# Optimization experiments

Measured on AMD Instinct MI355X. Metric: run time of the kernel, lower is better.

The kernel has to match this reference:

```python
import jax, jax.numpy as jnp
import numpy as np

N_NODES = 100000


def gcn_conv(x, W, b, row, col, n_nodes):
    # Symmetric GCN normalization without self-loops (add_self_loops=False):
    # deg[i] = number of incoming edges at target i (edge_weight = 1)
    deg = jax.ops.segment_sum(jnp.ones(row.shape[0], dtype=x.dtype), col,
                              num_segments=n_nodes)
    dinv = jnp.where(deg > 0, jax.lax.rsqrt(jnp.maximum(deg, 1.0)), 0.0)
    norm = dinv[row] * dinv[col]  # [E]
    h = x @ W                      # [N, out] linear transform first (PyG order)
    msg = h[row] * norm[:, None]   # gather + scale, [E, out]
    out = jax.ops.segment_sum(msg, col, num_segments=n_nodes)  # scatter-add
    return out + b


def setup_inputs() -> dict:
    key = jax.random.key(0)
    k1, k2, k3, k4, k5, k6 = jax.random.split(key, 6)
    n, in_c, hid, out_c, e = N_NODES, 128, 32, 16, 3200000
    x = jax.random.normal(k1, (n, in_c), dtype=jnp.float32)
    edge_index = jax.random.randint(k2, (2, e), 0, n, dtype=jnp.int64)
    # Glorot-style init for GCN weights, zeros bias (PyG default)
    W1 = jax.random.normal(k3, (in_c, hid), dtype=jnp.float32) / np.sqrt(in_c)
    b1 = jnp.zeros((hid,), dtype=jnp.float32)
    W2 = jax.random.normal(k4, (hid, out_c), dtype=jnp.float32) / np.sqrt(hid)
    b2 = jnp.zeros((out_c,), dtype=jnp.float32)
    return {"x": x, "edge_index": edge_index, "W1": W1, "b1": b1,
            "W2": W2, "b2": b2}


def reference(x, edge_index, W1, b1, W2, b2):
    row, col = edge_index[0], edge_index[1]
    h = gcn_conv(x, W1, b1, row, col, N_NODES)
    h = jax.nn.relu(h)
    out = gcn_conv(h, W2, b2, row, col, N_NODES)
    return (out, 0)
```

## Files before the change

kernel.cpp:

```cpp
#include <hip/hip_runtime.h>


#define WAVE 64
#define BN2 512
#define NBMAX 256
#define CHUNK 8192

typedef _Float16 f16;

__global__ void bucket_count_kernel(const int* __restrict__ col, int* __restrict__ gcnt,
                                    int E, int nb) {
    __shared__ int h[NBMAX];
    for (int i = threadIdx.x; i < nb; i += blockDim.x) h[i] = 0;
    __syncthreads();
    for (int e = blockIdx.x * blockDim.x + threadIdx.x; e < E; e += gridDim.x * blockDim.x)
        atomicAdd(&h[col[e] >> 9], 1);
    __syncthreads();
    for (int i = threadIdx.x; i < nb; i += blockDim.x)
        if (h[i]) atomicAdd(&gcnt[i], h[i]);
}

__global__ void bucket_scan_kernel(const int* __restrict__ cnt, int* __restrict__ bptr,
                                   int* __restrict__ gcur, int nb, int* __restrict__ gpcur,
                                   f16* __restrict__ hA, f16* __restrict__ h2t, int nzr) {
    int lane = threadIdx.x;
    if (lane == 0) gpcur[0] = 0;
    if (lane < 32)      hA[(size_t)nzr * 32 + lane]         = (f16)0.f;
    else if (lane < 48) h2t[(size_t)nzr * 16 + (lane - 32)] = (f16)0.f;
    int carry = 0;
    for (int base = 0; base < nb; base += WAVE) {
        int i = base + lane;
        int orig = (i < nb) ? cnt[i] : 0;
        int v = orig;
#pragma unroll
        for (int off = 1; off < WAVE; off <<= 1) {
            int t = __shfl_up(v, off, WAVE);
            if (lane >= off) v += t;
        }
        if (i < nb) { bptr[i] = carry + v - orig; gcur[i] = carry + v - orig; }
        carry += __shfl(v, WAVE - 1, WAVE);
    }
    if (lane == 0) bptr[nb] = carry;
}

__global__ void __launch_bounds__(512)
partition_kernel(const int* __restrict__ row, const int* __restrict__ col,
                 int* __restrict__ gcursor, unsigned* __restrict__ packed,
                 int E, int nb) {
    __shared__ int hist[NBMAX], excl[NBMAX], cursor[NBMAX], baseoff[NBMAX];
    __shared__ unsigned stage[CHUNK];
    int chunk0 = blockIdx.x * CHUNK;
    int cn = E - chunk0; if (cn > CHUNK) cn = CHUNK;
    for (int i = threadIdx.x; i < nb; i += blockDim.x) hist[i] = 0;
    __syncthreads();
    for (int i = threadIdx.x; i < cn; i += blockDim.x)
        atomicAdd(&hist[col[chunk0 + i] >> 9], 1);
    __syncthreads();
    if (threadIdx.x < WAVE) {
        int lane = threadIdx.x, carry = 0;
        for (int base = 0; base < nb; base += WAVE) {
            int i = base + lane;
            int orig = (i < nb) ? hist[i] : 0;
            int v = orig;
#pragma unroll
            for (int off = 1; off < WAVE; off <<= 1) {
                int t = __shfl_up(v, off, WAVE);
                if (lane >= off) v += t;
            }
            if (i < nb) { excl[i] = carry + v - orig; cursor[i] = carry + v - orig; }
            carry += __shfl(v, WAVE - 1, WAVE);
        }
    }
    __syncthreads();
    for (int b = threadIdx.x; b < nb; b += blockDim.x) {
        int c = hist[b];
        baseoff[b] = c ? atomicAdd(&gcursor[b], c) : 0;
    }
    __syncthreads();
    for (int i = threadIdx.x; i < cn; i += blockDim.x) {
        int c = col[chunk0 + i], r = row[chunk0 + i];
        int b = c >> 9;
        int pos = atomicAdd(&cursor[b], 1);
        stage[pos] = ((unsigned)r << 9) | (unsigned)(c & (BN2 - 1));
    }
    __syncthreads();
    int wave = threadIdx.x >> 6, lane = threadIdx.x & 63, nw = blockDim.x >> 6;
    for (int b = wave; b < nb; b += nw) {
        int c = hist[b]; if (!c) continue;
        int s = excl[b], d = baseoff[b];
        for (int k = lane; k < c; k += WAVE) packed[d + k] = stage[s + k];
    }
}

__global__ void __launch_bounds__(512)
sort_kernel(const int* __restrict__ bptr, const unsigned* __restrict__ packed,
            int* __restrict__ srcs, int2* __restrict__ pse,
            float* __restrict__ dinv, int* __restrict__ gpcur,
            int n, int nb, int E) {
    __shared__ int hist[BN2], pex[BN2], cur[BN2];
    __shared__ int pbase_s;
    int b = blockIdx.x;
    int start = bptr[b], end = bptr[b + 1];
    for (int i = threadIdx.x; i < BN2; i += blockDim.x) { hist[i] = 0; cur[i] = 0; }
    __syncthreads();
    for (int k = start + threadIdx.x; k < end; k += blockDim.x)
        atomicAdd(&hist[packed[k] & (BN2 - 1)], 1);
    __syncthreads();
    if (threadIdx.x < WAVE) {
        int lane = threadIdx.x, carry = 0;
#pragma unroll
        for (int base = 0; base < BN2; base += WAVE) {
            int i = base + lane;
            int pd = (hist[i] + 15) & ~15;
            int v = pd;
#pragma unroll
            for (int off = 1; off < WAVE; off <<= 1) {
                int t = __shfl_up(v, off, WAVE);
                if (lane >= off) v += t;
            }
            pex[i] = carry + v - pd;
            carry += __shfl(v, WAVE - 1, WAVE);
        }
        if (lane == 0) pbase_s = atomicAdd(gpcur, carry);
    }
    __syncthreads();
    int pbase = pbase_s;
    for (int i = threadIdx.x; i < BN2; i += blockDim.x) {
        int node = b * BN2 + i;
        if (node < n) {
            int d = hist[i], pd = (d + 15) & ~15;
            int ps = pbase + pex[i];
            pse[node]  = d ? make_int2(ps, ps + pd) : make_int2(0, 0);
            dinv[node] = d ? rsqrtf((float)d) : 0.f;
            for (int k = d; k < pd; ++k) srcs[ps + k] = n;
        }
    }
    __syncthreads();
    for (int k = start + threadIdx.x; k < end; k += blockDim.x) {
        unsigned p = packed[k];
        int lc = p & (BN2 - 1);
        int pos = atomicAdd(&cur[lc], 1);
        srcs[pbase + pex[lc] + pos] = (int)(p >> 9);
    }
}

template <int INC, int OUTC, int JT>
__global__ void __launch_bounds__(256, 4)
dense_kernel(const float* __restrict__ x, const float* __restrict__ W,
             const float* __restrict__ dinv, f16* __restrict__ h, int n) {
    const int LSTR = INC + 4;
    const int SP   = 256 / JT;
    const int NT   = SP * 2;
    __shared__ float Wt[OUTC * LSTR];
    for (int i = threadIdx.x; i < INC * OUTC; i += 256) {
        int k = i / OUTC, j = i % OUTC;
        Wt[j * LSTR + k] = W[i];
    }
    __syncthreads();
    const int jg = threadIdx.x % JT;
    const int sp = threadIdx.x / JT;
    int base = blockIdx.x * NT;
    int n0 = base + sp;
    int n1 = base + sp + SP;
    int n0c = n0 < n ? n0 : n - 1;
    int n1c = n1 < n ? n1 : n - 1;
    const float4* xr0 = (const float4*)(x + (size_t)n0c * INC);
    const float4* xr1 = (const float4*)(x + (size_t)n1c * INC);
    float a[2][4] = {{0.f, 0.f, 0.f, 0.f}, {0.f, 0.f, 0.f, 0.f}};
#pragma unroll 4
    for (int k4 = 0; k4 < INC / 4; ++k4) {
        float4 v0 = xr0[k4];
        float4 v1 = xr1[k4];
#pragma unroll
        for (int u = 0; u < 4; ++u) {
            float4 w = *(const float4*)(Wt + (jg + u * JT) * LSTR + 4 * k4);
            a[0][u] = fmaf(v0.x, w.x, fmaf(v0.y, w.y, fmaf(v0.z, w.z, fmaf(v0.w, w.w, a[0][u]))));
            a[1][u] = fmaf(v1.x, w.x, fmaf(v1.y, w.y, fmaf(v1.z, w.z, fmaf(v1.w, w.w, a[1][u]))));
        }
    }
#pragma unroll
    for (int pair = 0; pair < 2; ++pair) {
        int nn = pair ? n1 : n0;
        if (nn < n) {
            float d = dinv[nn];
            f16* hr = h + (size_t)nn * OUTC;
#pragma unroll
            for (int u = 0; u < 4; ++u) hr[jg + u * JT] = (f16)(a[pair][u] * d);
        }
    }
}

#define GLD32(s) (*(const f16*)(hb + (((unsigned)(s) << 6) + j2)))

template <bool RELU>
__global__ void __launch_bounds__(256)
csr_agg32x2_kernel(const int2* __restrict__ pse, const int* __restrict__ srcs,
                   const float* __restrict__ dinv, const f16* __restrict__ hs,
                   const float* __restrict__ bias, float* __restrict__ out,
                   int ostride, int n) {
    int lane = threadIdx.x & 63;
    int wid  = threadIdx.x >> 6;
    int j  = lane & 31;
    int eo = lane >> 5;
    int n0 = ((int)blockIdx.x * 4 + wid) * 2;
    if (n0 >= n) return;
    int n1 = n0 + 1;
    bool v1 = n1 < n;
    int4 se = *(const int4*)(pse + n0);
    int nb0 = (se.y - se.x) >> 3;
    int nb1 = v1 ? ((se.w - se.z) >> 3) : 0;
    float dv0 = dinv[n0];
    float dv1 = v1 ? dinv[n1] : 0.f;
    float bj = bias[j];
    size_t ob0 = (size_t)n0 * ostride + j;
    size_t ob1 = (size_t)n1 * ostride + j;
    int MAXB = nb0 > nb1 ? nb0 : nb1;
    if (MAXB == 0) {
        float v = bj;
        if (RELU) v = v > 0.f ? v : 0.f;
        if (eo == 0) out[ob0] = v;
        else if (v1) out[ob1] = v;
        return;
    }
    const unsigned j2 = (unsigned)(j << 1);
    const char* hb = (const char*)hs;
    const int4* P0 = (const int4*)(srcs + se.x) + eo;
    const int4* P1 = (const int4*)(srcs + (v1 ? se.z : se.x)) + eo;
    int nc0 = nb0 > 1 ? nb0 : 1;
    int nc1 = nb1 > 1 ? nb1 : 1;
    int4 sA0 = P0[0];
    int4 sA1 = P1[0];
    f16 h0 = GLD32(sA0.x), h1 = GLD32(sA0.y), h2 = GLD32(sA0.z), h3 = GLD32(sA0.w);
    f16 h4 = GLD32(sA1.x), h5 = GLD32(sA1.y), h6 = GLD32(sA1.z), h7 = GLD32(sA1.w);
    int4 sB0 = P0[(nc0 > 1 ? 1 : 0) * 2];
    int4 sB1 = P1[(nc1 > 1 ? 1 : 0) * 2];
    float acc0 = 0.f, acc1 = 0.f, acc2 = 0.f, acc3 = 0.f;
    for (int b = 0; b < MAXB - 1; ++b) {
        f16 g0 = GLD32(sB0.x), g1 = GLD32(sB0.y), g2 = GLD32(sB0.z), g3 = GLD32(sB0.w);
        f16 g4 = GLD32(sB1.x), g5 = GLD32(sB1.y), g6 = GLD32(sB1.z), g7 = GLD32(sB1.w);
        int x0 = (b + 2) < nc0 ? (b + 2) : nc0 - 1;
        int x1 = (b + 2) < nc1 ? (b + 2) : nc1 - 1;
        int4 t0 = P0[x0 * 2];
        int4 t1 = P1[x1 * 2];
        float m0 = b < nb0 ? 1.f : 0.f;
        float m1 = b < nb1 ? 1.f : 0.f;
        acc0 = fmaf(m0, (float)h0, acc0);
        acc1 = fmaf(m0, (float)h1, acc1);
        acc0 = fmaf(m0, (float)h2, acc0);
        acc1 = fmaf(m0, (float)h3, acc1);
        acc2 = fmaf(m1, (float)h4, acc2);
        acc3 = fmaf(m1, (float)h5, acc3);
        acc2 = fmaf(m1, (float)h6, acc2);
        acc3 = fmaf(m1, (float)h7, acc3);
        h0 = g0; h1 = g1; h2 = g2; h3 = g3;
        h4 = g4; h5 = g5; h6 = g6; h7 = g7;
        sB0 = t0; sB1 = t1;
    }
    {
        float m0 = (MAXB - 1) < nb0 ? 1.f : 0.f;
        float m1 = (MAXB - 1) < nb1 ? 1.f : 0.f;
        acc0 = fmaf(m0, (float)h0, acc0);
        acc1 = fmaf(m0, (float)h1, acc1);
        acc0 = fmaf(m0, (float)h2, acc0);
        acc1 = fmaf(m0, (float)h3, acc1);
        acc2 = fmaf(m1, (float)h4, acc2);
        acc3 = fmaf(m1, (float)h5, acc3);
        acc2 = fmaf(m1, (float)h6, acc2);
        acc3 = fmaf(m1, (float)h7, acc3);
    }
    float accA = acc0 + acc1;
    float accB = acc2 + acc3;
    accA += __shfl_xor(accA, 32, WAVE);
    accB += __shfl_xor(accB, 32, WAVE);
    if (eo == 0) {
        float v = accA * dv0 + bj;
        if (RELU) v = v > 0.f ? v : 0.f;
        out[ob0] = v;
    } else if (v1) {
        float v = accB * dv1 + bj;
        if (RELU) v = v > 0.f ? v : 0.f;
        out[ob1] = v;
    }
}

#define GLD16(s) (*(const f16*)(hb + (((unsigned)(s) << 5) + j2)))

template <bool RELU>
__global__ void __launch_bounds__(256)
csr_agg16x2_kernel(const int2* __restrict__ pse, const int* __restrict__ srcs,
                   const float* __restrict__ dinv, const f16* __restrict__ hs,
                   const float* __restrict__ bias, float* __restrict__ out,
                   int ostride, int n, int tailidx) {
    int bid = blockIdx.x;
    int lane = threadIdx.x & 63;
    int wid  = threadIdx.x >> 6;
    int j  = lane & 15;
    int eo = lane >> 4;
    if (tailidx >= 0 && bid == 0 && threadIdx.x == 0) out[tailidx] = 0.f;
    int n0 = (bid * 4 + wid) * 2;
    if (n0 >= n) return;
    int n1 = n0 + 1;
    bool v1 = n1 < n;
    int4 se = *(const int4*)(pse + n0);
    int nb0 = (se.y - se.x) >> 4;
    int nb1 = v1 ? ((se.w - se.z) >> 4) : 0;
    float dv0 = dinv[n0];
    float dv1 = v1 ? dinv[n1] : 0.f;
    float bj = bias[j];
    size_t ob0 = (size_t)n0 * ostride + j;
    size_t ob1 = (size_t)n1 * ostride + j;
    int MAXB = nb0 > nb1 ? nb0 : nb1;
    if (MAXB == 0) {
        float v = bj;
        if (RELU) v = v > 0.f ? v : 0.f;
        if (eo == 0) out[ob0] = v;
        else if (eo == 1 && v1) out[ob1] = v;
        return;
    }
    const unsigned j2 = (unsigned)(j << 1);
    const char* hb = (const char*)hs;
    const int4* P0 = (const int4*)(srcs + se.x) + eo;
    const int4* P1 = (const int4*)(srcs + (v1 ? se.z : se.x)) + eo;
    int nc0 = nb0 > 1 ? nb0 : 1;
    int nc1 = nb1 > 1 ? nb1 : 1;
    int4 sA0 = P0[0];
    int4 sA1 = P1[0];
    f16 h0 = GLD16(sA0.x), h1 = GLD16(sA0.y), h2 = GLD16(sA0.z), h3 = GLD16(sA0.w);
    f16 h4 = GLD16(sA1.x), h5 = GLD16(sA1.y), h6 = GLD16(sA1.z), h7 = GLD16(sA1.w);
    int4 sB0 = P0[(nc0 > 1 ? 1 : 0) * 4];
    int4 sB1 = P1[(nc1 > 1 ? 1 : 0) * 4];
    float acc0 = 0.f, acc1 = 0.f, acc2 = 0.f, acc3 = 0.f;
    for (int b = 0; b < MAXB - 1; ++b) {
        f16 g0 = GLD16(sB0.x), g1 = GLD16(sB0.y), g2 = GLD16(sB0.z), g3 = GLD16(sB0.w);
        f16 g4 = GLD16(sB1.x), g5 = GLD16(sB1.y), g6 = GLD16(sB1.z), g7 = GLD16(sB1.w);
        int x0 = (b + 2) < nc0 ? (b + 2) : nc0 - 1;
        int x1 = (b + 2) < nc1 ? (b + 2) : nc1 - 1;
        int4 t0 = P0[x0 * 4];
        int4 t1 = P1[x1 * 4];
        float m0 = b < nb0 ? 1.f : 0.f;
        float m1 = b < nb1 ? 1.f : 0.f;
        acc0 = fmaf(m0, (float)h0, acc0);
        acc1 = fmaf(m0, (float)h1, acc1);
        acc0 = fmaf(m0, (float)h2, acc0);
        acc1 = fmaf(m0, (float)h3, acc1);
        acc2 = fmaf(m1, (float)h4, acc2);
        acc3 = fmaf(m1, (float)h5, acc3);
        acc2 = fmaf(m1, (float)h6, acc2);
        acc3 = fmaf(m1, (float)h7, acc3);
        h0 = g0; h1 = g1; h2 = g2; h3 = g3;
        h4 = g4; h5 = g5; h6 = g6; h7 = g7;
        sB0 = t0; sB1 = t1;
    }
    {
        float m0 = (MAXB - 1) < nb0 ? 1.f : 0.f;
        float m1 = (MAXB - 1) < nb1 ? 1.f : 0.f;
        acc0 = fmaf(m0, (float)h0, acc0);
        acc1 = fmaf(m0, (float)h1, acc1);
        acc0 = fmaf(m0, (float)h2, acc0);
        acc1 = fmaf(m0, (float)h3, acc1);
        acc2 = fmaf(m1, (float)h4, acc2);
        acc3 = fmaf(m1, (float)h5, acc3);
        acc2 = fmaf(m1, (float)h6, acc2);
        acc3 = fmaf(m1, (float)h7, acc3);
    }
    float accA = acc0 + acc1;
    float accB = acc2 + acc3;
    accA += __shfl_xor(accA, 16, WAVE);
    accA += __shfl_xor(accA, 32, WAVE);
    accB += __shfl_xor(accB, 16, WAVE);
    accB += __shfl_xor(accB, 32, WAVE);
    if (eo == 0) {
        float v = accA * dv0 + bj;
        if (RELU) v = v > 0.f ? v : 0.f;
        out[ob0] = v;
    } else if (eo == 1 && v1) {
        float v = accB * dv1 + bj;
        if (RELU) v = v > 0.f ? v : 0.f;
        out[ob1] = v;
    }
}

extern "C" void kernel_launch(void* const* d_in, const int* in_sizes, int n_in,
                              void* d_out, int out_size, void* d_ws, size_t ws_size,
                              hipStream_t stream) {
    const float* x  = (const float*)d_in[0];
    const int*   ei = (const int*)d_in[1];
    const float* W1 = (const float*)d_in[2];
    const float* b1 = (const float*)d_in[3];
    const float* W2 = (const float*)d_in[4];
    const float* b2 = (const float*)d_in[5];

    const int IN_C = 128, HID = 32, OC = 16;
    const int N = in_sizes[0] / IN_C;
    const int E = in_sizes[1] / 2;
    const int* row = ei;
    const int* col = ei + E;
    const int NB = (N + BN2 - 1) / BN2;

    char* base = (char*)d_ws;
    size_t off = 0;
    auto carve = [&](size_t bytes) -> char* {
        char* p = base + off;
        off = (off + bytes + 255) & ~(size_t)255;
        return p;
    };
    int*      gcnt  = (int*)     carve((size_t)NB * 4);
    int*      bptr  = (int*)     carve((size_t)(NB + 1) * 4);
    int*      gcur  = (int*)     carve((size_t)NB * 4);
    int*      gpcur = (int*)     carve(8);
    float*    dinv  = (float*)   carve((size_t)N * 4);
    int2*     pse   = (int2*)    carve((size_t)(N + 2) * 8);
    unsigned* packed= (unsigned*)carve((size_t)E * 4);
    int*      srcsP = (int*)     carve(((size_t)E + (size_t)N * 32 + 256) * 4);
    f16*      hA    = (f16*)     carve((size_t)(N + 1) * 32 * 2);
    f16*      h2t   = (f16*)     carve((size_t)(N + 1) * 16 * 2);
    float*    bufB  = (float*)   carve((size_t)N * HID * 4);
    (void)ws_size; (void)n_in;

    float* outp = (float*)d_out;

    hipMemsetAsync(gcnt, 0, (size_t)NB * 4, stream);
    bucket_count_kernel<<<512, 256, 0, stream>>>(col, gcnt, E, NB);
    bucket_scan_kernel<<<1, 64, 0, stream>>>(gcnt, bptr, gcur, NB, gpcur, hA, h2t, N);
    partition_kernel<<<(E + CHUNK - 1) / CHUNK, 512, 0, stream>>>(row, col, gcur, packed, E, NB);
    sort_kernel<<<NB, 512, 0, stream>>>(bptr, packed, srcsP, pse, dinv, gpcur, N, NB, E);

    int npb = 8;
    int g2  = (N + npb - 1) / npb;

    {
        const int NT = (256 / 8) * 2;
        dense_kernel<128, 32, 8><<<(N + NT - 1) / NT, 256, 0, stream>>>(x, W1, dinv, hA, N);
        csr_agg32x2_kernel<true><<<g2, 256, 0, stream>>>(
            pse, srcsP, dinv, hA, b1, bufB, HID, N);
    }
    {
        const int NT = (256 / 4) * 2;
        dense_kernel<32, 16, 4><<<(N + NT - 1) / NT, 256, 0, stream>>>(bufB, W2, dinv, h2t, N);
        int tailidx = (out_size > N * OC) ? (N * OC) : -1;
        csr_agg16x2_kernel<false><<<g2, 256, 0, stream>>>(
            pse, srcsP, dinv, h2t, b2, outp, OC, N, tailidx);
    }
}
```

Baseline: 182.3 us.

## Split layer-1 aggregation into two source-half passes for gather locality

The sort kernel now splits each destination's neighbour list by source index (below or above N/2), padding each half separately, and emits three CSR range arrays: low half, high half and full. Layer-1 aggregation runs as two passes. The first writes partial sums over low-half sources, and the second adds the high-half sources, then applies the scale, bias and ReLU. This halves the gathered feature working set per pass, likely to improve cache hit rates on the random gathers. In exchange it adds an extra launch, a read-modify-write of the output buffer, more padding entries, and more sort-kernel bookkeeping.

```diff
diff --git a/kernel.cpp b/kernel.cpp
--- a/kernel.cpp
+++ b/kernel.cpp
@@ -94,31 +94,37 @@
 
 __global__ void __launch_bounds__(512)
 sort_kernel(const int* __restrict__ bptr, const unsigned* __restrict__ packed,
-            int* __restrict__ srcs, int2* __restrict__ pse,
-            float* __restrict__ dinv, int* __restrict__ gpcur,
-            int n, int nb, int E) {
-    __shared__ int hist[BN2], pex[BN2], cur[BN2];
+            int* __restrict__ srcs, int2* __restrict__ pseA, int2* __restrict__ pseB,
+            int2* __restrict__ pseF, float* __restrict__ dinv, int* __restrict__ gpcur,
+            int n, int nb, int E, int half) {
+    __shared__ int hist[2 * BN2];
+    __shared__ int pex[BN2], pdl[BN2];
+    __shared__ int cur[2 * BN2];
     __shared__ int pbase_s;
     int b = blockIdx.x;
     int start = bptr[b], end = bptr[b + 1];
-    for (int i = threadIdx.x; i < BN2; i += blockDim.x) { hist[i] = 0; cur[i] = 0; }
-    __syncthreads();
-    for (int k = start + threadIdx.x; k < end; k += blockDim.x)
-        atomicAdd(&hist[packed[k] & (BN2 - 1)], 1);
+    for (int i = threadIdx.x; i < 2 * BN2; i += blockDim.x) { hist[i] = 0; cur[i] = 0; }
+    __syncthreads();
+    for (int k = start + threadIdx.x; k < end; k += blockDim.x) {
+        unsigned p = packed[k];
+        int lc = p & (BN2 - 1);
+        int hsel = ((int)(p >> 9) >= half) ? BN2 : 0;
+        atomicAdd(&hist[lc + hsel], 1);
+    }
     __syncthreads();
     if (threadIdx.x < WAVE) {
         int lane = threadIdx.x, carry = 0;
 #pragma unroll
         for (int base = 0; base < BN2; base += WAVE) {
             int i = base + lane;
-            int pd = (hist[i] + 15) & ~15;
-            int v = pd;
+            int rg = ((hist[i] + 15) & ~15) + ((hist[i + BN2] + 15) & ~15);
+            int v = rg;
 #pragma unroll
             for (int off = 1; off < WAVE; off <<= 1) {
                 int t = __shfl_up(v, off, WAVE);
                 if (lane >= off) v += t;
             }
-            pex[i] = carry + v - pd;
+            pex[i] = carry + v - rg;
             carry += __shfl(v, WAVE - 1, WAVE);
         }
         if (lane == 0) pbase_s = atomicAdd(gpcur, carry);
@@ -128,19 +134,27 @@
     for (int i = threadIdx.x; i < BN2; i += blockDim.x) {
         int node = b * BN2 + i;
         if (node < n) {
-            int d = hist[i], pd = (d + 15) & ~15;
+            int dlo = hist[i], dhi = hist[i + BN2];
+            int pdlo = (dlo + 15) & ~15, pdhi = (dhi + 15) & ~15;
+            int d = dlo + dhi;
             int ps = pbase + pex[i];
-            pse[node]  = d ? make_int2(ps, ps + pd) : make_int2(0, 0);
+            pdl[i] = pdlo;
+            pseA[node] = d ? make_int2(ps, ps + pdlo) : make_int2(0, 0);
+            pseB[node] = d ? make_int2(ps + pdlo, ps + pdlo + pdhi) : make_int2(0, 0);
+            pseF[node] = d ? make_int2(ps, ps + pdlo + pdhi) : make_int2(0, 0);
             dinv[node] = d ? rsqrtf((float)d) : 0.f;
-            for (int k = d; k < pd; ++k) srcs[ps + k] = n;
+            for (int k = dlo; k < pdlo; ++k) srcs[ps + k] = n;
+            for (int k = dhi; k < pdhi; ++k) srcs[ps + pdlo + k] = n;
         }
     }
     __syncthreads();
     for (int k = start + threadIdx.x; k < end; k += blockDim.x) {
         unsigned p = packed[k];
         int lc = p & (BN2 - 1);
-        int pos = atomicAdd(&cur[lc], 1);
-        srcs[pbase + pex[lc] + pos] = (int)(p >> 9);
+        int src = (int)(p >> 9);
+        int h = src >= half;
+        int pos = atomicAdd(&cur[lc + (h ? BN2 : 0)], 1);
+        srcs[pbase + pex[lc] + (h ? pdl[lc] : 0) + pos] = src;
     }
 }
 
@@ -192,7 +206,7 @@
 
 #define GLD32(s) (*(const f16*)(hb + (((unsigned)(s) << 6) + j2)))
 
-template <bool RELU>
+template <int MODE>
 __global__ void __launch_bounds__(256)
 csr_agg32x2_kernel(const int2* __restrict__ pse, const int* __restrict__ srcs,
                    const float* __restrict__ dinv, const f16* __restrict__ hs,
@@ -216,10 +230,18 @@
     size_t ob1 = (size_t)n1 * ostride + j;
     int MAXB = nb0 > nb1 ? nb0 : nb1;
     if (MAXB == 0) {
-        float v = bj;
-        if (RELU) v = v > 0.f ? v : 0.f;
-        if (eo == 0) out[ob0] = v;
-        else if (v1) out[ob1] = v;
+        if (MODE == 0) {
+            if (eo == 0) out[ob0] = 0.f;
+            else if (v1) out[ob1] = 0.f;
+        } else {
+            if (eo == 0) {
+                float v = out[ob0] * dv0 + bj;
+                out[ob0] = v > 0.f ? v : 0.f;
+            } else if (v1) {
+                float v = out[ob1] * dv1 + bj;
+                out[ob1] = v > 0.f ? v : 0.f;
+            }
+        }
         return;
     }
     const unsigned j2 = (unsigned)(j << 1);
@@ -273,13 +295,17 @@
     accA += __shfl_xor(accA, 32, WAVE);
     accB += __shfl_xor(accB, 32, WAVE);
     if (eo == 0) {
-        float v = accA * dv0 + bj;
-        if (RELU) v = v > 0.f ? v : 0.f;
-        out[ob0] = v;
+        if (MODE == 0) out[ob0] = accA;
+        else {
+            float v = (out[ob0] + accA) * dv0 + bj;
+            out[ob0] = v > 0.f ? v : 0.f;
+        }
     } else if (v1) {
-        float v = accB * dv1 + bj;
-        if (RELU) v = v > 0.f ? v : 0.f;
-        out[ob1] = v;
+        if (MODE == 0) out[ob1] = accB;
+        else {
+            float v = (out[ob1] + accB) * dv1 + bj;
+            out[ob1] = v > 0.f ? v : 0.f;
+        }
     }
 }
 
@@ -409,7 +435,9 @@
     int*      gcur  = (int*)     carve((size_t)NB * 4);
     int*      gpcur = (int*)     carve(8);
     float*    dinv  = (float*)   carve((size_t)N * 4);
-    int2*     pse   = (int2*)    carve((size_t)(N + 2) * 8);
+    int2*     pseA  = (int2*)    carve((size_t)(N + 2) * 8);
+    int2*     pseB  = (int2*)    carve((size_t)(N + 2) * 8);
+    int2*     pseF  = (int2*)    carve((size_t)(N + 2) * 8);
     unsigned* packed= (unsigned*)carve((size_t)E * 4);
     int*      srcsP = (int*)     carve(((size_t)E + (size_t)N * 32 + 256) * 4);
     f16*      hA    = (f16*)     carve((size_t)(N + 1) * 32 * 2);
@@ -423,7 +451,8 @@
     bucket_count_kernel<<<512, 256, 0, stream>>>(col, gcnt, E, NB);
     bucket_scan_kernel<<<1, 64, 0, stream>>>(gcnt, bptr, gcur, NB, gpcur, hA, h2t, N);
     partition_kernel<<<(E + CHUNK - 1) / CHUNK, 512, 0, stream>>>(row, col, gcur, packed, E, NB);
-    sort_kernel<<<NB, 512, 0, stream>>>(bptr, packed, srcsP, pse, dinv, gpcur, N, NB, E);
+    sort_kernel<<<NB, 512, 0, stream>>>(bptr, packed, srcsP, pseA, pseB, pseF, dinv,
+                                        gpcur, N, NB, E, N / 2);
 
     int npb = 8;
     int g2  = (N + npb - 1) / npb;
@@ -431,14 +460,16 @@
     {
         const int NT = (256 / 8) * 2;
         dense_kernel<128, 32, 8><<<(N + NT - 1) / NT, 256, 0, stream>>>(x, W1, dinv, hA, N);
-        csr_agg32x2_kernel<true><<<g2, 256, 0, stream>>>(
-            pse, srcsP, dinv, hA, b1, bufB, HID, N);
+        csr_agg32x2_kernel<0><<<g2, 256, 0, stream>>>(
+            pseA, srcsP, dinv, hA, b1, bufB, HID, N);
+        csr_agg32x2_kernel<1><<<g2, 256, 0, stream>>>(
+            pseB, srcsP, dinv, hA, b1, bufB, HID, N);
     }
     {
         const int NT = (256 / 4) * 2;
         dense_kernel<32, 16, 4><<<(N + NT - 1) / NT, 256, 0, stream>>>(bufB, W2, dinv, h2t, N);
         int tailidx = (out_size > N * OC) ? (N * OC) : -1;
         csr_agg16x2_kernel<false><<<g2, 256, 0, stream>>>(
-            pse, srcsP, dinv, h2t, b2, outp, OC, N, tailidx);
-    }
-}
+            pseF, srcsP, dinv, h2t, b2, outp, OC, N, tailidx);
+    }
+}
```

Measured after the change: 202.8 us. 1.11x slower.
